# Kernel tuning notes

Measured on AMD Instinct MI355X. Metric: run time of the kernel, lower is better.

Reference implementation:

```python
import jax, jax.numpy as jnp
import numpy as np

N = 50000
E = 800000
IN_C = 128
HID = 16
HEADS = 8
OUT_C = 128
NEG_SLOPE = 0.2
EPS = 1e-16


def setup_inputs() -> dict:
    key = jax.random.key(0)
    ks = jax.random.split(key, 12)
    x = jax.random.normal(ks[0], (N, IN_C), dtype=jnp.float32)
    edge_index = jax.random.randint(ks[1], (2, E), 0, N, dtype=jnp.int32)
    s1 = 1.0 / np.sqrt(IN_C)
    s2 = 1.0 / np.sqrt(HID * HEADS)
    W1 = jax.random.normal(ks[2], (IN_C, HEADS * HID), dtype=jnp.float32) * s1
    att_src1 = jax.random.normal(ks[3], (HEADS, HID), dtype=jnp.float32) * s1
    att_dst1 = jax.random.normal(ks[4], (HEADS, HID), dtype=jnp.float32) * s1
    b1 = jnp.zeros((HEADS * HID,), dtype=jnp.float32)
    W2 = jax.random.normal(ks[5], (HEADS * HID, OUT_C), dtype=jnp.float32) * s2
    att_src2 = jax.random.normal(ks[6], (1, OUT_C), dtype=jnp.float32) * s2
    att_dst2 = jax.random.normal(ks[7], (1, OUT_C), dtype=jnp.float32) * s2
    b2 = jnp.zeros((OUT_C,), dtype=jnp.float32)
    return {"x": x, "edge_index": edge_index, "W1": W1, "att_src1": att_src1,
            "att_dst1": att_dst1, "b1": b1, "W2": W2, "att_src2": att_src2,
            "att_dst2": att_dst2, "b2": b2}


def _add_self_loops(edge_index, n):
    loop = jnp.arange(n, dtype=edge_index.dtype)
    src = jnp.concatenate([edge_index[0], loop])
    dst = jnp.concatenate([edge_index[1], loop])
    return src, dst


def gat_conv(x, src, dst, W, att_src, att_dst, bias, heads, out_c, concat):
    n = x.shape[0]
    h = (x @ W).reshape(n, heads, out_c)          # [N, H, C]
    a_src = jnp.einsum('nhc,hc->nh', h, att_src)  # [N, H]
    a_dst = jnp.einsum('nhc,hc->nh', h, att_dst)
    e = a_src[src] + a_dst[dst]                   # [E', H]
    e = jax.nn.leaky_relu(e, NEG_SLOPE)
    # segment softmax over edges grouped by destination node
    m = jax.ops.segment_max(e, dst, num_segments=n)          # [N, H]
    m = jnp.where(jnp.isfinite(m), m, 0.0)
    ex = jnp.exp(e - m[dst])                                  # [E', H]
    denom = jax.ops.segment_sum(ex, dst, num_segments=n)      # [N, H]
    alpha = ex / (denom[dst] + EPS)                            # [E', H]
    msg = alpha[:, :, None] * h[src]                           # [E', H, C]
    out = jax.ops.segment_sum(msg, dst, num_segments=n)       # [N, H, C]
    if concat:
        out = out.reshape(n, heads * out_c)
    else:
        out = out.mean(axis=1)
    return out + bias


def reference(x, edge_index, W1, att_src1, att_dst1, b1, W2, att_src2, att_dst2, b2):
    src, dst = _add_self_loops(edge_index, N)
    h = gat_conv(x, src, dst, W1, att_src1, att_dst1, b1, HEADS, HID, True)
    h = jax.nn.relu(h)
    # dropout is identity in eval mode
    out = gat_conv(h, src, dst, W2, att_src2, att_dst2, b2, 1, OUT_C, False)
    return out
```

## Files before the change

kernel.cpp:

```cpp
#include <hip/hip_runtime.h>


constexpr int N_NODES = 50000;
constexpr int E_EDGES = 800000;
constexpr int ETOT = E_EDGES + N_NODES;
constexpr float NEG_SLOPE = 0.2f;
constexpr float EPS = 1e-16f;
constexpr int SCAN_BLK = 512;
constexpr int NBLK_SCAN = (N_NODES + SCAN_BLK - 1) / SCAN_BLK;

typedef short bf16x8 __attribute__((ext_vector_type(8)));
typedef float f32x4 __attribute__((ext_vector_type(4)));

__device__ __forceinline__ float lrelu(float x) { return x > 0.f ? x : NEG_SLOPE * x; }
__device__ __forceinline__ ushort f2bf(float f) {
    uint u = __float_as_uint(f);
    return (ushort)((u + 0x7fffu + ((u >> 16) & 1u)) >> 16);
}
__device__ __forceinline__ float bf2f(uint u) { return __uint_as_float(u << 16); }

__device__ __forceinline__ void fma8(float* acc, uint4 p, float w, float& ws) {
    ws += w;
    acc[0] += w * bf2f(p.x & 0xffffu); acc[1] += w * bf2f(p.x >> 16);
    acc[2] += w * bf2f(p.y & 0xffffu); acc[3] += w * bf2f(p.y >> 16);
    acc[4] += w * bf2f(p.z & 0xffffu); acc[5] += w * bf2f(p.z >> 16);
    acc[6] += w * bf2f(p.w & 0xffffu); acc[7] += w * bf2f(p.w >> 16);
}

__global__ __launch_bounds__(256) void convert_W(const float* __restrict__ W1,
                                                 const float* __restrict__ W2,
                                                 const float* __restrict__ attS2,
                                                 const float* __restrict__ attD2,
                                                 ushort* __restrict__ W1t,
                                                 ushort* __restrict__ W2t,
                                                 float* __restrict__ vs,
                                                 float* __restrict__ vd,
                                                 uint* __restrict__ cnt16) {
    const int t = threadIdx.x;
    if (blockIdx.x >= 2) {
        const int i = (blockIdx.x - 2) * 256 + t;
        if (i < (N_NODES + 1) / 2) cnt16[i] = 0;
        return;
    }
    const float* W = (blockIdx.x == 0) ? W1 : W2;
    ushort* Wt = (blockIdx.x == 0) ? W1t : W2t;
    const int n = t >> 1, k0 = (t & 1) * 64;
    for (int k = 0; k < 64; k += 2) {
        uint lo = f2bf(W[(size_t)(k0 + k) * 128 + n]);
        uint hi = f2bf(W[(size_t)(k0 + k + 1) * 128 + n]);
        *(uint*)&Wt[(size_t)n * 128 + k0 + k] = lo | (hi << 16);
    }
    if (blockIdx.x == 1) {
        const int k = t & 127;
        const float* av = (t < 128) ? attS2 : attD2;
        float* dst = (t < 128) ? vs : vd;
        float s = 0.f;
        for (int c = 0; c < 128; ++c) s += W2[(size_t)k * 128 + c] * av[c];
        dst[k] = s;
    }
}

__device__ __forceinline__ uint cnt_at(const uint* cnt16, int i) {
    return (cnt16[i >> 1] >> ((i & 1) * 16)) & 0xffffu;
}

__global__ __launch_bounds__(SCAN_BLK) void block_sums(const uint* __restrict__ cnt16,
                                                       int* __restrict__ bsum) {
    __shared__ int sm[SCAN_BLK];
    int i = blockIdx.x * SCAN_BLK + threadIdx.x;
    sm[threadIdx.x] = (i < N_NODES) ? (int)cnt_at(cnt16, i) : 0;
    __syncthreads();
    for (int off = SCAN_BLK / 2; off > 0; off >>= 1) {
        if (threadIdx.x < off) sm[threadIdx.x] += sm[threadIdx.x + off];
        __syncthreads();
    }
    if (threadIdx.x == 0) bsum[blockIdx.x] = sm[0];
}

__global__ __launch_bounds__(SCAN_BLK) void scan_final_fused(const uint* __restrict__ cnt16,
                                                             const int* __restrict__ bsum,
                                                             int* __restrict__ rowptr) {
    __shared__ int sb[128];
    __shared__ int sm[SCAN_BLK];
    const int t = threadIdx.x;
    if (t < 128) sb[t] = (t < NBLK_SCAN) ? bsum[t] : 0;
    __syncthreads();
    for (int off = 1; off < 128; off <<= 1) {
        int v = 0;
        if (t < 128 && t >= off) v = sb[t - off];
        __syncthreads();
        if (t < 128) sb[t] += v;
        __syncthreads();
    }
    const int bid = blockIdx.x;
    const int bpre = sb[bid] - bsum[bid];

    const int i = bid * SCAN_BLK + t;
    const int v = (i < N_NODES) ? (int)cnt_at(cnt16, i) : 0;
    sm[t] = v;
    __syncthreads();
    for (int off = 1; off < SCAN_BLK; off <<= 1) {
        int x = (t >= off) ? sm[t - off] : 0;
        __syncthreads();
        sm[t] += x;
        __syncthreads();
    }
    if (i < N_NODES) rowptr[i] = bpre + sm[t] - v;
    if (bid == 0 && t == 0) rowptr[N_NODES] = ETOT;
}

__global__ __launch_bounds__(256) void scatter_kernel(const int* __restrict__ ei,
                                                      const int* __restrict__ rowptr,
                                                      const ushort* __restrict__ rank,
                                                      int* __restrict__ csrc) {
    int e = blockIdx.x * blockDim.x + threadIdx.x;
    if (e >= ETOT) return;
    int s, d;
    if (e < E_EDGES) { s = ei[e]; d = ei[E_EDGES + e]; }
    else             { s = d = e - E_EDGES; }
    const int pos = rowptr[d] + (int)rank[e];
    __builtin_nontemporal_store(s, &csrc[pos]);
}

template <bool BF16IN, bool ATT8, bool ATTIN>
__global__ __launch_bounds__(256) void mfma_gemm(const void* __restrict__ Xv,
                                                 const ushort* __restrict__ Wt,
                                                 ushort* __restrict__ H,
                                                 const float* __restrict__ attS,
                                                 const float* __restrict__ attD,
                                                 float* __restrict__ aS,
                                                 float* __restrict__ aD,
                                                 const int* __restrict__ ei,
                                                 uint* __restrict__ cnt16,
                                                 ushort* __restrict__ rank,
                                                 int cblocks, int nrows) {
    __shared__ __align__(16) char smem[16384 + 32768];
    ushort* lx = (ushort*)smem;
    ushort* lw = (ushort*)(smem + 16384);
    float*  hs = (float*)smem;

    const int t = threadIdx.x;

    if (blockIdx.x < cblocks) {
        const int e = blockIdx.x * 256 + t;
        if (e < ETOT) {
            const int d = (e < E_EDGES) ? ei[E_EDGES + e] : (e - E_EDGES);
            const uint shift = (d & 1) * 16;
            const uint old = atomicAdd(&cnt16[d >> 1], 1u << shift);
            rank[e] = (ushort)((old >> shift) & 0xffffu);
        }
        return;
    }

    const int r0 = (blockIdx.x - cblocks) * 64;

    {
        const int n = t >> 1, half = t & 1;
        const ushort* src = Wt + (size_t)n * 128 + half * 64;
        #pragma unroll
        for (int c = 0; c < 8; ++c) {
            int cx = half * 8 + c;
            uint4 v = *(const uint4*)(src + c * 8);
            *(uint4*)&lw[(n * 16 + (cx ^ (n & 7))) * 8] = v;
        }
    }
    {
        const int r = t >> 2, q = t & 3;
        const int grow = r0 + r;
        const uint4 z = {0, 0, 0, 0};
        #pragma unroll
        for (int cc = 0; cc < 4; ++cc) {
            int cx = q * 4 + cc;
            uint4 packed = z;
            if (grow < nrows) {
                if (BF16IN) {
                    packed = *(const uint4*)((const ushort*)Xv + (size_t)grow * 128 + cx * 8);
                } else {
                    const float* X = (const float*)Xv;
                    const float4 f0 = *(const float4*)(X + (size_t)grow * 128 + cx * 8);
                    const float4 f1 = *(const float4*)(X + (size_t)grow * 128 + cx * 8 + 4);
                    packed.x = (uint)f2bf(f0.x) | ((uint)f2bf(f0.y) << 16);
                    packed.y = (uint)f2bf(f0.z) | ((uint)f2bf(f0.w) << 16);
                    packed.z = (uint)f2bf(f1.x) | ((uint)f2bf(f1.y) << 16);
                    packed.w = (uint)f2bf(f1.z) | ((uint)f2bf(f1.w) << 16);
                }
            }
            *(uint4*)&lx[(r * 16 + (cx ^ (r & 7))) * 8] = packed;
        }
    }
    __syncthreads();

    const int wv = t >> 6, l = t & 63;
    const int row = wv * 16 + (l & 15);
    const int lg = l >> 4;
    f32x4 acc[8] = {};

    #pragma unroll
    for (int kb = 0; kb < 4; ++kb) {
        const int cx = kb * 4 + lg;
        bf16x8 a = *(const bf16x8*)&lx[(row * 16 + (cx ^ (row & 7))) * 8];
        #pragma unroll
        for (int nt = 0; nt < 8; ++nt) {
            const int n = nt * 16 + (l & 15);
            bf16x8 b = *(const bf16x8*)&lw[(n * 16 + (cx ^ (n & 7))) * 8];
            acc[nt] = __builtin_amdgcn_mfma_f32_16x16x32_bf16(a, b, acc[nt], 0, 0, 0);
        }
    }

    #pragma unroll
    for (int reg = 0; reg < 4; ++reg) {
        const int grow = r0 + wv * 16 + lg * 4 + reg;
        if (grow < nrows) {
            #pragma unroll
            for (int nt = 0; nt < 8; ++nt)
                H[(size_t)grow * 128 + nt * 16 + (l & 15)] = f2bf(acc[nt][reg]);
        }
    }

    if (ATT8) {
        __syncthreads();
        #pragma unroll
        for (int reg = 0; reg < 4; ++reg) {
            const int r = wv * 16 + lg * 4 + reg;
            #pragma unroll
            for (int nt = 0; nt < 8; ++nt)
                hs[r * 130 + nt * 16 + (l & 15)] = acc[nt][reg];
        }
        __syncthreads();
        for (int q = t; q < 512; q += 256) {
            const int r = q >> 3, h = q & 7;
            if (r0 + r < nrows) {
                float sv = 0.f, dv = 0.f;
                #pragma unroll
                for (int j = 0; j < 16; ++j) {
                    const float hv = hs[r * 130 + h * 16 + j];
                    sv += hv * attS[h * 16 + j];
                    dv += hv * attD[h * 16 + j];
                }
                aS[(size_t)(r0 + r) * 8 + h] = sv;
                aD[(size_t)(r0 + r) * 8 + h] = dv;
            }
        }
    }

    if (ATTIN) {
        const int r = t >> 2, qq = t & 3;
        float ps = 0.f, pd = 0.f;
        #pragma unroll
        for (int cc = 0; cc < 4; ++cc) {
            const int cx = qq * 4 + cc;
            const uint4 p = *(const uint4*)&lx[(r * 16 + (cx ^ (r & 7))) * 8];
            const uint w[4] = {p.x, p.y, p.z, p.w};
            #pragma unroll
            for (int q = 0; q < 4; ++q) {
                const float e0 = bf2f(w[q] & 0xffffu);
                const float e1 = bf2f(w[q] >> 16);
                ps += e0 * attS[cx * 8 + 2 * q] + e1 * attS[cx * 8 + 2 * q + 1];
                pd += e0 * attD[cx * 8 + 2 * q] + e1 * attD[cx * 8 + 2 * q + 1];
            }
        }
        ps += __shfl_xor(ps, 1); ps += __shfl_xor(ps, 2);
        pd += __shfl_xor(pd, 1); pd += __shfl_xor(pd, 2);
        if (qq == 0 && r0 + r < nrows) { aS[r0 + r] = ps; aD[r0 + r] = pd; }
    }
}

#define GISSUE(P, JJ)                                                          \
    {                                                                          \
        const int jx_ = (JJ);                                                  \
        const int sx_ = __shfl(s_l, jx_ & 63);                                 \
        P = zero4;                                                             \
        if (jx_ < rem) P = *(const uint4*)(Hm + (size_t)sx_ * 128 + i * 8);    \
    }

__global__ __launch_bounds__(256) void agg8(const int* __restrict__ rowptr,
                                            const int* __restrict__ csrc,
                                            const float* __restrict__ aS,
                                            const float* __restrict__ aD,
                                            const ushort* __restrict__ Hm,
                                            const float* __restrict__ bias,
                                            ushort* __restrict__ o1bf) {
    __shared__ float wlds[4][512];
    const int wv = threadIdx.x >> 6;
    const int d = blockIdx.x * 4 + wv;
    const int lane = threadIdx.x & 63;
    const int g = lane >> 4, i = lane & 15, hc = i >> 1;
    const int hw = lane & 7;
    const float adh = aD[(size_t)d * 8 + hw];

    const int base = rowptr[d], end = rowptr[d + 1];
    float acc[8] = {0.f, 0.f, 0.f, 0.f, 0.f, 0.f, 0.f, 0.f};
    float ws = 0.f;
    const uint4 zero4 = {0, 0, 0, 0};

    for (int c0 = base; c0 < end; c0 += 64) {
        const int rem = min(64, end - c0);
        const int s_l = (lane < rem) ? csrc[c0 + lane] : 0;

        uint4 p0, p1, p2, p3;
        GISSUE(p0, g); GISSUE(p1, g + 4); GISSUE(p2, g + 8); GISSUE(p3, g + 12);

        const int nwc = (rem + 7) >> 3;
        for (int jj = 0; jj < nwc; ++jj) {
            const int j = jj * 8 + (lane >> 3);
            const int sj = __shfl(s_l, j & 63);
            float w = 0.f;
            if (j < rem) w = __expf(lrelu(aS[(size_t)sj * 8 + hw] + adh));
            wlds[wv][j * 8 + hw] = w;
        }

        const int niter = (rem + 3) >> 2;
        for (int tb = 0; tb < niter; tb += 4) {
            const int j0 = 4 * tb + g;
            {
                const float w = (j0 < rem) ? wlds[wv][j0 * 8 + hc] : 0.f;
                fma8(acc, p0, w, ws);
                GISSUE(p0, j0 + 16);
            }
            {
                const int j1 = j0 + 4;
                const float w = (j1 < rem) ? wlds[wv][j1 * 8 + hc] : 0.f;
                fma8(acc, p1, w, ws);
                GISSUE(p1, j1 + 16);
            }
            {
                const int j2 = j0 + 8;
                const float w = (j2 < rem) ? wlds[wv][j2 * 8 + hc] : 0.f;
                fma8(acc, p2, w, ws);
                GISSUE(p2, j2 + 16);
            }
            {
                const int j3 = j0 + 12;
                const float w = (j3 < rem) ? wlds[wv][j3 * 8 + hc] : 0.f;
                fma8(acc, p3, w, ws);
                GISSUE(p3, j3 + 16);
            }
        }
    }

    #pragma unroll
    for (int k = 0; k < 8; ++k) {
        acc[k] += __shfl_xor(acc[k], 16);
        acc[k] += __shfl_xor(acc[k], 32);
    }
    ws += __shfl_xor(ws, 16);
    ws += __shfl_xor(ws, 32);

    if (g == 0) {
        const float inv = 1.f / (ws + EPS);
        float v[8];
        #pragma unroll
        for (int k = 0; k < 8; ++k) v[k] = fmaxf(acc[k] * inv + bias[i * 8 + k], 0.f);
        uint4 pk;
        pk.x = (uint)f2bf(v[0]) | ((uint)f2bf(v[1]) << 16);
        pk.y = (uint)f2bf(v[2]) | ((uint)f2bf(v[3]) << 16);
        pk.z = (uint)f2bf(v[4]) | ((uint)f2bf(v[5]) << 16);
        pk.w = (uint)f2bf(v[6]) | ((uint)f2bf(v[7]) << 16);
        *(uint4*)(o1bf + (size_t)d * 128 + i * 8) = pk;
    }
}

__global__ __launch_bounds__(256) void agg1(const int* __restrict__ rowptr,
                                            const int* __restrict__ csrc,
                                            const float* __restrict__ aS,
                                            const float* __restrict__ aD,
                                            const ushort* __restrict__ Hm,
                                            const float* __restrict__ bias,
                                            float* __restrict__ out) {
    const int wv = threadIdx.x >> 6;
    const int d = blockIdx.x * 4 + wv;
    const int lane = threadIdx.x & 63;
    const int g = lane >> 4, i = lane & 15;
    const float ad = aD[d];

    const int base = rowptr[d], end = rowptr[d + 1];
    float acc[8] = {0.f, 0.f, 0.f, 0.f, 0.f, 0.f, 0.f, 0.f};
    float ws = 0.f;
    const uint4 zero4 = {0, 0, 0, 0};

    for (int c0 = base; c0 < end; c0 += 64) {
        const int rem = min(64, end - c0);
        const int s_l = (lane < rem) ? csrc[c0 + lane] : 0;

        uint4 p0, p1, p2, p3;
        GISSUE(p0, g); GISSUE(p1, g + 4); GISSUE(p2, g + 8); GISSUE(p3, g + 12);

        const float w_l = (lane < rem) ? __expf(lrelu(aS[s_l] + ad)) : 0.f;

        const int niter = (rem + 3) >> 2;
        for (int tb = 0; tb < niter; tb += 4) {
            const int j0 = 4 * tb + g;
            {
                const float wr = __shfl(w_l, j0 & 63);
                const float w = (j0 < rem) ? wr : 0.f;
                fma8(acc, p0, w, ws);
                GISSUE(p0, j0 + 16);
            }
            {
                const int j1 = j0 + 4;
                const float wr = __shfl(w_l, j1 & 63);
                const float w = (j1 < rem) ? wr : 0.f;
                fma8(acc, p1, w, ws);
                GISSUE(p1, j1 + 16);
            }
            {
                const int j2 = j0 + 8;
                const float wr = __shfl(w_l, j2 & 63);
                const float w = (j2 < rem) ? wr : 0.f;
                fma8(acc, p2, w, ws);
                GISSUE(p2, j2 + 16);
            }
            {
                const int j3 = j0 + 12;
                const float wr = __shfl(w_l, j3 & 63);
                const float w = (j3 < rem) ? wr : 0.f;
                fma8(acc, p3, w, ws);
                GISSUE(p3, j3 + 16);
            }
        }
    }

    #pragma unroll
    for (int k = 0; k < 8; ++k) {
        acc[k] += __shfl_xor(acc[k], 16);
        acc[k] += __shfl_xor(acc[k], 32);
    }
    ws += __shfl_xor(ws, 16);
    ws += __shfl_xor(ws, 32);

    if (g == 0) {
        const float inv = 1.f / (ws + EPS);
        float4 o0, o1v;
        o0.x = acc[0] * inv + bias[i * 8 + 0];
        o0.y = acc[1] * inv + bias[i * 8 + 1];
        o0.z = acc[2] * inv + bias[i * 8 + 2];
        o0.w = acc[3] * inv + bias[i * 8 + 3];
        o1v.x = acc[4] * inv + bias[i * 8 + 4];
        o1v.y = acc[5] * inv + bias[i * 8 + 5];
        o1v.z = acc[6] * inv + bias[i * 8 + 6];
        o1v.w = acc[7] * inv + bias[i * 8 + 7];
        *(float4*)(out + (size_t)d * 128 + i * 8) = o0;
        *(float4*)(out + (size_t)d * 128 + i * 8 + 4) = o1v;
    }
}

extern "C" void kernel_launch(void* const* d_in, const int* in_sizes, int n_in,
                              void* d_out, int out_size, void* d_ws, size_t ws_size,
                              hipStream_t stream) {
    const float* x        = (const float*)d_in[0];
    const int*   ei       = (const int*)  d_in[1];
    const float* W1       = (const float*)d_in[2];
    const float* att_src1 = (const float*)d_in[3];
    const float* att_dst1 = (const float*)d_in[4];
    const float* b1       = (const float*)d_in[5];
    const float* W2       = (const float*)d_in[6];
    const float* att_src2 = (const float*)d_in[7];
    const float* att_dst2 = (const float*)d_in[8];
    const float* b2       = (const float*)d_in[9];
    float* out = (float*)d_out;

    ushort* Hbf  = (ushort*)d_ws;
    ushort* o1bf = Hbf + (size_t)N_NODES * 128;
    float*  aS1  = (float*)(o1bf + (size_t)N_NODES * 128);
    float*  aD1  = aS1 + (size_t)N_NODES * 8;
    float*  aS2  = aD1 + (size_t)N_NODES * 8;
    float*  aD2  = aS2 + N_NODES;
    float*  vs   = aD2 + N_NODES;
    float*  vd   = vs + 128;
    ushort* W1t  = (ushort*)(vd + 128);
    ushort* W2t  = W1t + 128 * 128;
    uint* cnt16  = (uint*)(W2t + 128 * 128);
    int* rowptr  = (int*)(cnt16 + (N_NODES + 1) / 2 + 1);
    int* bsum    = rowptr + N_NODES + 1;
    ushort* rank = (ushort*)(bsum + 128);
    int* csrc    = (int*)(rank + ETOT + 2);

    const int zblk = ((N_NODES + 1) / 2 + 255) / 256;
    const int eblk = (ETOT + 255) / 256;
    const int gemm_blocks = (N_NODES + 63) / 64;
    const int agg_blocks = N_NODES / 4;

    convert_W<<<2 + zblk, 256, 0, stream>>>(W1, W2, att_src2, att_dst2,
                                            W1t, W2t, vs, vd, cnt16);

    mfma_gemm<false, true, false><<<eblk + gemm_blocks, 256, 0, stream>>>(
        x, W1t, Hbf, att_src1, att_dst1, aS1, aD1, ei, cnt16, rank, eblk, N_NODES);

    block_sums<<<NBLK_SCAN, SCAN_BLK, 0, stream>>>(cnt16, bsum);
    scan_final_fused<<<NBLK_SCAN, SCAN_BLK, 0, stream>>>(cnt16, bsum, rowptr);
    scatter_kernel<<<eblk, 256, 0, stream>>>(ei, rowptr, rank, csrc);

    agg8<<<agg_blocks, 256, 0, stream>>>(rowptr, csrc, aS1, aD1, Hbf, b1, o1bf);

    mfma_gemm<true, false, true><<<gemm_blocks, 256, 0, stream>>>(
        o1bf, W2t, Hbf, vs, vd, aS2, aD2, nullptr, nullptr, nullptr, 0, N_NODES);

    agg1<<<agg_blocks, 256, 0, stream>>>(rowptr, csrc, aS2, aD2, Hbf, b2, out);
}
```

Baseline: 216.6 us.

## Split edge counting from GEMM and deepen gather prefetch ring to six

Moves the per-edge atomic counting and ranking out of the first GEMM launch into a separate count_rank kernel. The layer-1 GEMM is now launched after the CSR build, right before aggregation, which may keep H in cache for agg8. Both aggregation kernels replace the four-register gather prefetch with a six-entry unrolled ring, putting more loads in flight per wave. The cost is one extra kernel launch, the overlap lost between atomics and GEMM, and higher register pressure in the aggregation kernels.

```diff
diff --git a/kernel.cpp b/kernel.cpp
--- a/kernel.cpp
+++ b/kernel.cpp
@@ -60,6 +60,17 @@
     }
 }
 
+__global__ __launch_bounds__(256) void count_rank(const int* __restrict__ ei,
+                                                  uint* __restrict__ cnt16,
+                                                  ushort* __restrict__ rank) {
+    int e = blockIdx.x * blockDim.x + threadIdx.x;
+    if (e >= ETOT) return;
+    int d = (e < E_EDGES) ? ei[E_EDGES + e] : (e - E_EDGES);
+    const uint shift = (d & 1) * 16;
+    uint old = atomicAdd(&cnt16[d >> 1], 1u << shift);
+    rank[e] = (ushort)((old >> shift) & 0xffffu);
+}
+
 __device__ __forceinline__ uint cnt_at(const uint* cnt16, int i) {
     return (cnt16[i >> 1] >> ((i & 1) * 16)) & 0xffffu;
 }
@@ -130,29 +141,14 @@
                                                  const float* __restrict__ attD,
                                                  float* __restrict__ aS,
                                                  float* __restrict__ aD,
-                                                 const int* __restrict__ ei,
-                                                 uint* __restrict__ cnt16,
-                                                 ushort* __restrict__ rank,
-                                                 int cblocks, int nrows) {
+                                                 int nrows) {
     __shared__ __align__(16) char smem[16384 + 32768];
     ushort* lx = (ushort*)smem;
     ushort* lw = (ushort*)(smem + 16384);
     float*  hs = (float*)smem;
 
     const int t = threadIdx.x;
-
-    if (blockIdx.x < cblocks) {
-        const int e = blockIdx.x * 256 + t;
-        if (e < ETOT) {
-            const int d = (e < E_EDGES) ? ei[E_EDGES + e] : (e - E_EDGES);
-            const uint shift = (d & 1) * 16;
-            const uint old = atomicAdd(&cnt16[d >> 1], 1u << shift);
-            rank[e] = (ushort)((old >> shift) & 0xffffu);
-        }
-        return;
-    }
-
-    const int r0 = (blockIdx.x - cblocks) * 64;
+    const int r0 = blockIdx.x * 64;
 
     {
         const int n = t >> 1, half = t & 1;
@@ -297,8 +293,9 @@
         const int rem = min(64, end - c0);
         const int s_l = (lane < rem) ? csrc[c0 + lane] : 0;
 
-        uint4 p0, p1, p2, p3;
-        GISSUE(p0, g); GISSUE(p1, g + 4); GISSUE(p2, g + 8); GISSUE(p3, g + 12);
+        uint4 ring[6];
+        #pragma unroll
+        for (int s = 0; s < 6; ++s) GISSUE(ring[s], 4 * s + g);
 
         const int nwc = (rem + 7) >> 3;
         for (int jj = 0; jj < nwc; ++jj) {
@@ -310,30 +307,15 @@
         }
 
         const int niter = (rem + 3) >> 2;
-        for (int tb = 0; tb < niter; tb += 4) {
-            const int j0 = 4 * tb + g;
-            {
-                const float w = (j0 < rem) ? wlds[wv][j0 * 8 + hc] : 0.f;
-                fma8(acc, p0, w, ws);
-                GISSUE(p0, j0 + 16);
-            }
-            {
-                const int j1 = j0 + 4;
-                const float w = (j1 < rem) ? wlds[wv][j1 * 8 + hc] : 0.f;
-                fma8(acc, p1, w, ws);
-                GISSUE(p1, j1 + 16);
-            }
-            {
-                const int j2 = j0 + 8;
-                const float w = (j2 < rem) ? wlds[wv][j2 * 8 + hc] : 0.f;
-                fma8(acc, p2, w, ws);
-                GISSUE(p2, j2 + 16);
-            }
-            {
-                const int j3 = j0 + 12;
-                const float w = (j3 < rem) ? wlds[wv][j3 * 8 + hc] : 0.f;
-                fma8(acc, p3, w, ws);
-                GISSUE(p3, j3 + 16);
+        for (int tb = 0; tb < niter; tb += 6) {
+            #pragma unroll
+            for (int s = 0; s < 6; ++s) {
+                if (tb + s < niter) {
+                    const int j = (tb + s) * 4 + g;
+                    const float w = (j < rem) ? wlds[wv][j * 8 + hc] : 0.f;
+                    fma8(acc, ring[s], w, ws);
+                    GISSUE(ring[s], j + 24);
+                }
             }
         }
     }
@@ -382,40 +364,23 @@
         const int rem = min(64, end - c0);
         const int s_l = (lane < rem) ? csrc[c0 + lane] : 0;
 
-        uint4 p0, p1, p2, p3;
-        GISSUE(p0, g); GISSUE(p1, g + 4); GISSUE(p2, g + 8); GISSUE(p3, g + 12);
+        uint4 ring[6];
+        #pragma unroll
+        for (int s = 0; s < 6; ++s) GISSUE(ring[s], 4 * s + g);
 
         const float w_l = (lane < rem) ? __expf(lrelu(aS[s_l] + ad)) : 0.f;
 
         const int niter = (rem + 3) >> 2;
-        for (int tb = 0; tb < niter; tb += 4) {
-            const int j0 = 4 * tb + g;
-            {
-                const float wr = __shfl(w_l, j0 & 63);
-                const float w = (j0 < rem) ? wr : 0.f;
-                fma8(acc, p0, w, ws);
-                GISSUE(p0, j0 + 16);
-            }
-            {
-                const int j1 = j0 + 4;
-                const float wr = __shfl(w_l, j1 & 63);
-                const float w = (j1 < rem) ? wr : 0.f;
-                fma8(acc, p1, w, ws);
-                GISSUE(p1, j1 + 16);
-            }
-            {
-                const int j2 = j0 + 8;
-                const float wr = __shfl(w_l, j2 & 63);
-                const float w = (j2 < rem) ? wr : 0.f;
-                fma8(acc, p2, w, ws);
-                GISSUE(p2, j2 + 16);
-            }
-            {
-                const int j3 = j0 + 12;
-                const float wr = __shfl(w_l, j3 & 63);
-                const float w = (j3 < rem) ? wr : 0.f;
-                fma8(acc, p3, w, ws);
-                GISSUE(p3, j3 + 16);
+        for (int tb = 0; tb < niter; tb += 6) {
+            #pragma unroll
+            for (int s = 0; s < 6; ++s) {
+                if (tb + s < niter) {
+                    const int j = (tb + s) * 4 + g;
+                    const float wr = __shfl(w_l, j & 63);
+                    const float w = (j < rem) ? wr : 0.f;
+                    fma8(acc, ring[s], w, ws);
+                    GISSUE(ring[s], j + 24);
+                }
             }
         }
     }
@@ -482,18 +447,16 @@
 
     convert_W<<<2 + zblk, 256, 0, stream>>>(W1, W2, att_src2, att_dst2,
                                             W1t, W2t, vs, vd, cnt16);
-
-    mfma_gemm<false, true, false><<<eblk + gemm_blocks, 256, 0, stream>>>(
-        x, W1t, Hbf, att_src1, att_dst1, aS1, aD1, ei, cnt16, rank, eblk, N_NODES);
-
+    count_rank<<<eblk, 256, 0, stream>>>(ei, cnt16, rank);
     block_sums<<<NBLK_SCAN, SCAN_BLK, 0, stream>>>(cnt16, bsum);
     scan_final_fused<<<NBLK_SCAN, SCAN_BLK, 0, stream>>>(cnt16, bsum, rowptr);
     scatter_kernel<<<eblk, 256, 0, stream>>>(ei, rowptr, rank, csrc);
 
+    mfma_gemm<false, true, false><<<gemm_blocks, 256, 0, stream>>>(
+        x, W1t, Hbf, att_src1, att_dst1, aS1, aD1, N_NODES);
     agg8<<<agg_blocks, 256, 0, stream>>>(rowptr, csrc, aS1, aD1, Hbf, b1, o1bf);
 
     mfma_gemm<true, false, true><<<gemm_blocks, 256, 0, stream>>>(
-        o1bf, W2t, Hbf, vs, vd, aS2, aD2, nullptr, nullptr, nullptr, 0, N_NODES);
-
+        o1bf, W2t, Hbf, vs, vd, aS2, aD2, N_NODES);
     agg1<<<agg_blocks, 256, 0, stream>>>(rowptr, csrc, aS2, aD2, Hbf, b2, out);
 }
```

After: 211.2 us. 2.5% less time.
